# Performance work log

Measured on AMD Instinct MI355X. Metric: run time of the kernel, lower is better.

The kernel has to match this reference:

```python
import jax, jax.numpy as jnp
import numpy as np

B, E, H, N_TAYLOR = 8192, 256, 4096, 4
BN_EPS = 1e-5


def setup_inputs() -> dict:
    key = jax.random.key(0)
    ks = jax.random.split(key, 6)
    s = 0.02
    return {
        "z1": jax.random.normal(ks[0], (B, E), jnp.float32),
        "z2": jax.random.normal(ks[1], (B, E), jnp.float32),
        "p1": jax.random.normal(ks[2], (B, E), jnp.float32),
        "p2": jax.random.normal(ks[3], (B, E), jnp.float32),
        "W1": jax.random.normal(ks[4], (E, H), jnp.float32) * s,
        "gamma": jnp.ones((H,), jnp.float32),
        "beta": jnp.zeros((H,), jnp.float32),
        "W2": jax.random.normal(ks[5], (H, E), jnp.float32) * s,
        "b2": jnp.zeros((E,), jnp.float32),
        "lamda_inv": jnp.asarray(100.0, jnp.float32),
    }


def _predictor(z, W1, gamma, beta, W2, b2):
    h = z @ W1                                   # [B, H]
    mu = jnp.mean(h, axis=0)
    var = jnp.mean(jnp.square(h - mu), axis=0)   # biased var (torch BN training)
    h = (h - mu) * jax.lax.rsqrt(var + BN_EPS) * gamma + beta
    h = jax.nn.relu(h)
    return h @ W2 + b2                           # [B, E]


def _l2norm(x):
    n = jnp.linalg.norm(x, axis=1, keepdims=True)
    return x / jnp.maximum(n, 1e-12)


def _mec(view1, view2, lamda_inv):
    v1, v2 = _l2norm(view1), _l2norm(view2)
    c = (v1 @ v2.T) / lamda_inv                  # [B, B]
    power = c
    sum_p = jnp.zeros_like(c)
    for k in range(1, N_TAYLOR + 1):
        if k > 1:
            power = power @ c
        sign = 1.0 if (k + 1) % 2 == 0 else -1.0
        sum_p = sum_p + sign * power / k
    return jnp.trace(sum_p)


def reference(z1, z2, p1, p2, W1, gamma, beta, W2, b2, lamda_inv):
    q1 = _predictor(z1, W1, gamma, beta, W2, b2)
    q2 = _predictor(z2, W1, gamma, beta, W2, b2)
    loss = (_mec(p1, q2, lamda_inv) + _mec(p2, q1, lamda_inv)) * 0.5 / B
    return -loss * lamda_inv
```

## Files before the change

### kernel.cpp

```cpp
#include <hip/hip_runtime.h>

#define B_ROWS 8192
#define E_DIM  256
#define H_DIM  4096

typedef __attribute__((ext_vector_type(8))) short short8;
typedef __attribute__((ext_vector_type(4))) float f32x4;

typedef __attribute__((address_space(1))) const void* gas1_t;
typedef __attribute__((address_space(3))) void*       las3_t;

__device__ __forceinline__ float b2f(unsigned short s) {
    return __uint_as_float(((unsigned)s) << 16);
}
__device__ __forceinline__ unsigned short f2b(float f) {
    unsigned u = __float_as_uint(f);
    u += 0x7fffu + ((u >> 16) & 1u);
    return (unsigned short)(u >> 16);
}

__device__ __forceinline__ int swz(int row, int slot) {
    return slot ^ ((row >> 1) & 3);
}

__global__ void k_transpose_cast(const float* __restrict__ in,
                                 unsigned short* __restrict__ out,
                                 int R, int C) {
    __shared__ float tile[32][33];
    const int c0 = blockIdx.x * 32, r0 = blockIdx.y * 32;
    const int tx = threadIdx.x & 31, ty = threadIdx.x >> 5;
#pragma unroll
    for (int j = 0; j < 4; ++j)
        tile[ty * 4 + j][tx] = in[(size_t)(r0 + ty * 4 + j) * C + c0 + tx];
    __syncthreads();
#pragma unroll
    for (int j = 0; j < 4; ++j)
        out[(size_t)(c0 + ty * 4 + j) * R + r0 + tx] = f2b(tile[tx][ty * 4 + j]);
}

__global__ void k_cast_bf16(const float* __restrict__ in,
                            unsigned short* __restrict__ out, int n4) {
    int i = blockIdx.x * blockDim.x + threadIdx.x;
    if (i < n4) {
        float4 v = ((const float4*)in)[i];
        ushort4 o;
        o.x = f2b(v.x); o.y = f2b(v.y); o.z = f2b(v.z); o.w = f2b(v.w);
        ((ushort4*)out)[i] = o;
    }
}

__global__ __launch_bounds__(256) void k_gemm1(
    const unsigned short* __restrict__ A, const unsigned short* __restrict__ Bt,
    unsigned short* __restrict__ Cout,
    float* __restrict__ cs, float* __restrict__ cs2,
    int M, int N, int K) {
    constexpr int BK = 32, BM = 128, BN = 128;
    constexpr int MI = 4, NI = 4;
    __shared__ __align__(16) short As[BM * BK];
    __shared__ __align__(16) short Bs[BN * BK];

    const int t = threadIdx.x;
    const int lane = t & 63, wv = t >> 6;
    const int wr = wv >> 1, wc = wv & 1;
    const int l15 = lane & 15, quad = lane >> 4;
    const int m0 = blockIdx.y * BM, n0 = blockIdx.x * BN;

    f32x4 acc[MI][NI] = {};

    for (int k0 = 0; k0 < K; k0 += BK) {
#pragma unroll
        for (int q = 0; q < 2; ++q) {
            int u = q * 256 + t;
            int row = u >> 2, kc = swz(row, u & 3);
            const short* gp = (const short*)A + (size_t)(m0 + row) * K + k0 + kc * 8;
            short* lp = As + (size_t)(q * 256 + (wv << 6)) * 8;
            __builtin_amdgcn_global_load_lds((gas1_t)gp, (las3_t)lp, 16, 0, 0);
        }
#pragma unroll
        for (int q = 0; q < 2; ++q) {
            int u = q * 256 + t;
            int row = u >> 2, kc = swz(row, u & 3);
            const short* gp = (const short*)Bt + (size_t)(n0 + row) * K + k0 + kc * 8;
            short* lp = Bs + (size_t)(q * 256 + (wv << 6)) * 8;
            __builtin_amdgcn_global_load_lds((gas1_t)gp, (las3_t)lp, 16, 0, 0);
        }
        __syncthreads();

        short8 af[MI], bfr[NI];
#pragma unroll
        for (int mi = 0; mi < MI; ++mi) {
            int row = wr * 64 + mi * 16 + l15;
            af[mi] = *(const short8*)(As + row * BK + (swz(row, quad) << 3));
        }
#pragma unroll
        for (int ni = 0; ni < NI; ++ni) {
            int row = wc * 64 + ni * 16 + l15;
            bfr[ni] = *(const short8*)(Bs + row * BK + (swz(row, quad) << 3));
        }
#pragma unroll
        for (int mi = 0; mi < MI; ++mi)
#pragma unroll
            for (int ni = 0; ni < NI; ++ni)
                acc[mi][ni] = __builtin_amdgcn_mfma_f32_16x16x32_bf16(
                    af[mi], bfr[ni], acc[mi][ni], 0, 0, 0);
        __syncthreads();
    }

#pragma unroll
    for (int ni = 0; ni < NI; ++ni) {
        float s = 0.f, s2 = 0.f;
#pragma unroll
        for (int mi = 0; mi < MI; ++mi)
#pragma unroll
            for (int r = 0; r < 4; ++r) {
                int row = m0 + wr * 64 + mi * 16 + quad * 4 + r;
                int col = n0 + wc * 64 + ni * 16 + l15;
                float v = acc[mi][ni][r];
                Cout[(size_t)row * N + col] = f2b(v);
                s += v; s2 += v * v;
            }
        s  += __shfl_xor(s, 16);  s  += __shfl_xor(s, 32);
        s2 += __shfl_xor(s2, 16); s2 += __shfl_xor(s2, 32);
        if (quad == 0) {
            int col = n0 + wc * 64 + ni * 16 + l15;
            atomicAdd(&cs[col], s);
            atomicAdd(&cs2[col], s2);
        }
    }
}

__global__ void k_bnprep(const float* __restrict__ sum, const float* __restrict__ sumsq,
                         const float* __restrict__ gamma, const float* __restrict__ beta,
                         float* __restrict__ scale, float* __restrict__ shift) {
    int j = blockIdx.x * 256 + threadIdx.x;
    float mu = sum[j] * (1.f / B_ROWS);
    float var = sumsq[j] * (1.f / B_ROWS) - mu * mu;
    float sc = gamma[j] * rsqrtf(var + 1e-5f);
    scale[j] = sc;
    shift[j] = beta[j] - mu * sc;
}

__global__ __launch_bounds__(256) void k_gemm2f(
    const unsigned short* __restrict__ A, const unsigned short* __restrict__ Bt,
    float* __restrict__ Cout, const float* __restrict__ bias,
    const float* __restrict__ scale, const float* __restrict__ shift,
    int M, int N, int K) {
    constexpr int BK = 32, BM = 64, BN = 128;
    constexpr int MI = 2, NI = 4;
    __shared__ __align__(16) short As[BM * BK];
    __shared__ __align__(16) short Bs[BN * BK];

    const int t = threadIdx.x;
    const int lane = t & 63, wv = t >> 6;
    const int wr = wv >> 1, wc = wv & 1;
    const int l15 = lane & 15, quad = lane >> 4;
    const int m0 = blockIdx.y * BM, n0 = blockIdx.x * BN;

    const int Kc = K / gridDim.z;
    const int kbeg = blockIdx.z * Kc, kend = kbeg + Kc;

    const int arow = t >> 2, akc = t & 3;
    const unsigned short* hp = A + (size_t)(m0 + arow) * K + akc * 8;
    short* awp = As + arow * BK + (swz(arow, akc) << 3);
    const float* scp = scale + akc * 8;
    const float* shp = shift + akc * 8;

    f32x4 acc[MI][NI] = {};

    uint4 hreg; float4 sc0, sc1, sh0, sh1;
    {
        hreg = *(const uint4*)(hp + kbeg);
        sc0 = *(const float4*)(scp + kbeg); sc1 = *(const float4*)(scp + kbeg + 4);
        sh0 = *(const float4*)(shp + kbeg); sh1 = *(const float4*)(shp + kbeg + 4);
    }

    for (int k0 = kbeg; k0 < kend; k0 += BK) {
#pragma unroll
        for (int q = 0; q < 2; ++q) {
            int u = q * 256 + t;
            int row = u >> 2, kc = swz(row, u & 3);
            const short* gp = (const short*)Bt + (size_t)(n0 + row) * K + k0 + kc * 8;
            short* lp = Bs + (size_t)(q * 256 + (wv << 6)) * 8;
            __builtin_amdgcn_global_load_lds((gas1_t)gp, (las3_t)lp, 16, 0, 0);
        }

        uint4 cur = hreg;
        float sarr[8] = {sc0.x, sc0.y, sc0.z, sc0.w, sc1.x, sc1.y, sc1.z, sc1.w};
        float harr[8] = {sh0.x, sh0.y, sh0.z, sh0.w, sh1.x, sh1.y, sh1.z, sh1.w};
        if (k0 + BK < kend) {
            hreg = *(const uint4*)(hp + k0 + BK);
            sc0 = *(const float4*)(scp + k0 + BK); sc1 = *(const float4*)(scp + k0 + BK + 4);
            sh0 = *(const float4*)(shp + k0 + BK); sh1 = *(const float4*)(shp + k0 + BK + 4);
        }
        const unsigned short* hu = (const unsigned short*)&cur;
        short8 packed;
#pragma unroll
        for (int j = 0; j < 8; ++j) {
            float v = fmaxf(b2f(hu[j]) * sarr[j] + harr[j], 0.f);
            packed[j] = (short)f2b(v);
        }
        *(short8*)awp = packed;
        __syncthreads();

        short8 af[MI], bfr[NI];
#pragma unroll
        for (int mi = 0; mi < MI; ++mi) {
            int row = wr * 32 + mi * 16 + l15;
            af[mi] = *(const short8*)(As + row * BK + (swz(row, quad) << 3));
        }
#pragma unroll
        for (int ni = 0; ni < NI; ++ni) {
            int row = wc * 64 + ni * 16 + l15;
            bfr[ni] = *(const short8*)(Bs + row * BK + (swz(row, quad) << 3));
        }
#pragma unroll
        for (int mi = 0; mi < MI; ++mi)
#pragma unroll
            for (int ni = 0; ni < NI; ++ni)
                acc[mi][ni] = __builtin_amdgcn_mfma_f32_16x16x32_bf16(
                    af[mi], bfr[ni], acc[mi][ni], 0, 0, 0);
        __syncthreads();
    }

#pragma unroll
    for (int mi = 0; mi < MI; ++mi)
#pragma unroll
        for (int ni = 0; ni < NI; ++ni)
#pragma unroll
            for (int r = 0; r < 4; ++r) {
                int row = m0 + wr * 32 + mi * 16 + quad * 4 + r;
                int col = n0 + wc * 64 + ni * 16 + l15;
                float v = acc[mi][ni][r];
                if (blockIdx.z == 0) v += bias[col];
                atomicAdd(&Cout[(size_t)row * N + col], v);
            }
}

__global__ void k_rownorm4(const float* __restrict__ a0, const float* __restrict__ a1,
                           const float* __restrict__ a2, const float* __restrict__ a3,
                           float* __restrict__ o0, float* __restrict__ o1,
                           float* __restrict__ o2, float* __restrict__ o3) {
    int which = blockIdx.y;
    const float* x = which == 0 ? a0 : which == 1 ? a1 : which == 2 ? a2 : a3;
    float* inv = which == 0 ? o0 : which == 1 ? o1 : which == 2 ? o2 : o3;
    int row = blockIdx.x * 4 + (threadIdx.x >> 6);
    int lane = threadIdx.x & 63;
    float4 v = ((const float4*)(x + (size_t)row * E_DIM))[lane];
    float s = v.x * v.x + v.y * v.y + v.z * v.z + v.w * v.w;
#pragma unroll
    for (int o = 32; o; o >>= 1) s += __shfl_down(s, o);
    if (lane == 0) inv[row] = 1.f / fmaxf(sqrtf(s), 1e-12f);
}

__global__ void k_tn_cast(
    const float* __restrict__ x0, const float* __restrict__ x1,
    const float* __restrict__ x2, const float* __restrict__ x3,
    const float* __restrict__ i0, const float* __restrict__ i1,
    const float* __restrict__ i2, const float* __restrict__ i3,
    unsigned short* __restrict__ o0, unsigned short* __restrict__ o1,
    unsigned short* __restrict__ o2, unsigned short* __restrict__ o3) {
    const int z = blockIdx.z;
    const float* x = z == 0 ? x0 : z == 1 ? x1 : z == 2 ? x2 : x3;
    const float* inv = z == 0 ? i0 : z == 1 ? i1 : z == 2 ? i2 : i3;
    unsigned short* out = z == 0 ? o0 : z == 1 ? o1 : z == 2 ? o2 : o3;

    __shared__ float tile[32][33];
    const int c0 = blockIdx.x * 32, r0 = blockIdx.y * 32;
    const int tx = threadIdx.x & 31, ty = threadIdx.x >> 5;
#pragma unroll
    for (int j = 0; j < 4; ++j) {
        int r = r0 + ty * 4 + j;
        tile[ty * 4 + j][tx] = x[(size_t)r * E_DIM + c0 + tx] * inv[r];
    }
    __syncthreads();
#pragma unroll
    for (int j = 0; j < 4; ++j)
        out[(size_t)(c0 + ty * 4 + j) * B_ROWS + r0 + tx] = f2b(tile[tx][ty * 4 + j]);
}

#define GKS 16
__global__ __launch_bounds__(256) void k_gram(
    const unsigned short* __restrict__ p1T, const unsigned short* __restrict__ q2T,
    const unsigned short* __restrict__ p2T, const unsigned short* __restrict__ q1T,
    float* __restrict__ Ma, float* __restrict__ Mb) {
    constexpr int BK = 32;
    const int mec = blockIdx.z >> 4, kz = blockIdx.z & 15;
    const unsigned short* A = mec ? p2T : p1T;
    const unsigned short* Bt = mec ? q1T : q2T;
    float* Mout = mec ? Mb : Ma;

    __shared__ __align__(16) short As[64 * BK];
    __shared__ __align__(16) short Bs[64 * BK];

    const int t = threadIdx.x;
    const int lane = t & 63, wv = t >> 6;
    const int wr = wv >> 1, wc = wv & 1;
    const int l15 = lane & 15, quad = lane >> 4;
    const int m0 = blockIdx.y * 64, n0 = blockIdx.x * 64;
    const int kbeg = kz * (B_ROWS / GKS);

    f32x4 acc[2][2] = {};

    for (int k0 = kbeg; k0 < kbeg + B_ROWS / GKS; k0 += BK) {
        {
            int row = t >> 2, kc = swz(row, t & 3);
            const short* gpa = (const short*)A + (size_t)(m0 + row) * B_ROWS + k0 + kc * 8;
            short* lpa = As + (size_t)(wv << 6) * 8;
            __builtin_amdgcn_global_load_lds((gas1_t)gpa, (las3_t)lpa, 16, 0, 0);
            const short* gpb = (const short*)Bt + (size_t)(n0 + row) * B_ROWS + k0 + kc * 8;
            short* lpb = Bs + (size_t)(wv << 6) * 8;
            __builtin_amdgcn_global_load_lds((gas1_t)gpb, (las3_t)lpb, 16, 0, 0);
        }
        __syncthreads();

        short8 af[2], bfr[2];
#pragma unroll
        for (int mi = 0; mi < 2; ++mi) {
            int row = wr * 32 + mi * 16 + l15;
            af[mi] = *(const short8*)(As + row * BK + (swz(row, quad) << 3));
        }
#pragma unroll
        for (int ni = 0; ni < 2; ++ni) {
            int row = wc * 32 + ni * 16 + l15;
            bfr[ni] = *(const short8*)(Bs + row * BK + (swz(row, quad) << 3));
        }
#pragma unroll
        for (int mi = 0; mi < 2; ++mi)
#pragma unroll
            for (int ni = 0; ni < 2; ++ni)
                acc[mi][ni] = __builtin_amdgcn_mfma_f32_16x16x32_bf16(
                    af[mi], bfr[ni], acc[mi][ni], 0, 0, 0);
        __syncthreads();
    }

#pragma unroll
    for (int mi = 0; mi < 2; ++mi)
#pragma unroll
        for (int ni = 0; ni < 2; ++ni)
#pragma unroll
            for (int r = 0; r < 4; ++r) {
                int row = m0 + wr * 32 + mi * 16 + quad * 4 + r;
                int col = n0 + wc * 32 + ni * 16 + l15;
                atomicAdd(&Mout[(size_t)row * E_DIM + col], acc[mi][ni][r]);
            }
}

__global__ void k_m2(const float* __restrict__ Ma, const float* __restrict__ Mb,
                     float* __restrict__ M2a, float* __restrict__ M2b) {
    const float* M = blockIdx.z ? Mb : Ma;
    float* M2 = blockIdx.z ? M2b : M2a;
    int b = blockIdx.x * 16 + (threadIdx.x & 15);
    int a = blockIdx.y * 16 + (threadIdx.x >> 4);
    float s = 0.f;
    for (int k = 0; k < E_DIM; ++k) s += M[a * E_DIM + k] * M[k * E_DIM + b];
    M2[a * E_DIM + b] = s;
}

__global__ __launch_bounds__(256) void k_traces2(
    const float* __restrict__ Ma, const float* __restrict__ M2a,
    const float* __restrict__ Mb, const float* __restrict__ M2b,
    const float* __restrict__ lam, float* __restrict__ out) {
    const float* M  = blockIdx.z ? Mb  : Ma;
    const float* M2 = blockIdx.z ? M2b : M2a;
    const int i0 = blockIdx.y * 32, j0 = blockIdx.x * 32;
    const int t = threadIdx.x, col = t & 31, row = t >> 5;

    __shared__ float A[32][33], Bt[32][33], A2[32][33], B2[32][33];
#pragma unroll
    for (int r = 0; r < 4; ++r) {
        int rr = r * 8 + row;
        A [rr][col] = M [(i0 + rr) * E_DIM + j0 + col];
        Bt[rr][col] = M [(j0 + rr) * E_DIM + i0 + col];
        A2[rr][col] = M2[(i0 + rr) * E_DIM + j0 + col];
        B2[rr][col] = M2[(j0 + rr) * E_DIM + i0 + col];
    }
    __syncthreads();

    float lamv = lam[0];
    float il = 1.f / lamv;
    float F = -0.5f * lamv * (1.f / B_ROWS);
    float c1 = F * il;
    float c2 = -F * 0.5f * il * il;
    float c3 = F * (1.f / 3.f) * il * il * il;
    float c4 = -F * 0.25f * il * il * il * il;

    float s = 0.f;
#pragma unroll
    for (int r = 0; r < 4; ++r) {
        int rr = r * 8 + row;
        float mij = A[rr][col], mji = Bt[col][rr];
        float m2ij = A2[rr][col], m2ji = B2[col][rr];
        s += c2 * mij * mji + c3 * m2ij * mji + c4 * m2ij * m2ji;
        if (i0 + rr == j0 + col) s += c1 * mij;
    }
#pragma unroll
    for (int o = 32; o; o >>= 1) s += __shfl_down(s, o);
    __shared__ float red[4];
    if ((t & 63) == 0) red[t >> 6] = s;
    __syncthreads();
    if (t == 0) atomicAdd(out, red[0] + red[1] + red[2] + red[3]);
}

extern "C" void kernel_launch(void* const* d_in, const int* in_sizes, int n_in,
                              void* d_out, int out_size, void* d_ws, size_t ws_size,
                              hipStream_t stream) {
    const float* z1 = (const float*)d_in[0];
    const float* z2 = (const float*)d_in[1];
    const float* p1 = (const float*)d_in[2];
    const float* p2 = (const float*)d_in[3];
    const float* W1 = (const float*)d_in[4];
    const float* gamma = (const float*)d_in[5];
    const float* beta = (const float*)d_in[6];
    const float* W2 = (const float*)d_in[7];
    const float* b2 = (const float*)d_in[8];
    const float* lam = (const float*)d_in[9];
    float* out = (float*)d_out;
    char* ws = (char*)d_ws;

    size_t off = 0;
    auto alloc = [&](size_t bytes) { size_t o = off; off += (bytes + 255) & ~(size_t)255; return o; };
    unsigned short* W1T = (unsigned short*)(ws + alloc((size_t)E_DIM * H_DIM * 2));
    unsigned short* W2T = (unsigned short*)(ws + alloc((size_t)H_DIM * E_DIM * 2));
    unsigned short* zb  = (unsigned short*)(ws + alloc((size_t)B_ROWS * E_DIM * 2));
    unsigned short* h   = (unsigned short*)(ws + alloc((size_t)B_ROWS * H_DIM * 2));
    float* q1 = (float*)(ws + alloc((size_t)B_ROWS * E_DIM * 4));
    float* q2 = (float*)(ws + alloc((size_t)B_ROWS * E_DIM * 4));
    float* colsum   = (float*)(ws + alloc(H_DIM * 4));
    float* colsumsq = (float*)(ws + alloc(H_DIM * 4));
    float* scale = (float*)(ws + alloc(H_DIM * 4));
    float* shift = (float*)(ws + alloc(H_DIM * 4));
    float* invp1 = (float*)(ws + alloc(B_ROWS * 4));
    float* invp2 = (float*)(ws + alloc(B_ROWS * 4));
    float* invq1 = (float*)(ws + alloc(B_ROWS * 4));
    float* invq2 = (float*)(ws + alloc(B_ROWS * 4));
    float* Ma  = (float*)(ws + alloc((size_t)E_DIM * E_DIM * 4));
    float* Mb  = (float*)(ws + alloc((size_t)E_DIM * E_DIM * 4));
    float* M2a = (float*)(ws + alloc((size_t)E_DIM * E_DIM * 4));
    float* M2b = (float*)(ws + alloc((size_t)E_DIM * E_DIM * 4));

    const size_t TSZ = (size_t)E_DIM * B_ROWS;
    unsigned short* p1T = h;
    unsigned short* q2T = h + TSZ;
    unsigned short* p2T = h + 2 * TSZ;
    unsigned short* q1T = h + 3 * TSZ;

    hipMemsetAsync(out, 0, sizeof(float), stream);
    hipMemsetAsync(q1, 0, (size_t)2 * B_ROWS * E_DIM * sizeof(float), stream);

    k_transpose_cast<<<dim3(H_DIM / 32, E_DIM / 32), 256, 0, stream>>>(W1, W1T, E_DIM, H_DIM);
    k_transpose_cast<<<dim3(E_DIM / 32, H_DIM / 32), 256, 0, stream>>>(W2, W2T, H_DIM, E_DIM);

    const float* zs[2] = {z1, z2};
    float* qs[2] = {q1, q2};
    for (int v = 0; v < 2; ++v) {
        k_cast_bf16<<<dim3(B_ROWS * E_DIM / 4 / 256), 256, 0, stream>>>(zs[v], zb, B_ROWS * E_DIM / 4);
        hipMemsetAsync(colsum, 0, H_DIM * 2 * sizeof(float), stream);
        k_gemm1<<<dim3(H_DIM / 128, B_ROWS / 128), 256, 0, stream>>>(
            zb, W1T, h, colsum, colsumsq, B_ROWS, H_DIM, E_DIM);
        k_bnprep<<<dim3(H_DIM / 256), 256, 0, stream>>>(colsum, colsumsq, gamma, beta, scale, shift);
        k_gemm2f<<<dim3(E_DIM / 128, B_ROWS / 64, 4), 256, 0, stream>>>(
            h, W2T, qs[v], b2, scale, shift, B_ROWS, E_DIM, H_DIM);
    }

    k_rownorm4<<<dim3(B_ROWS / 4, 4), 256, 0, stream>>>(p1, p2, q1, q2, invp1, invp2, invq1, invq2);

    k_tn_cast<<<dim3(E_DIM / 32, B_ROWS / 32, 4), 256, 0, stream>>>(
        p1, q2, p2, q1, invp1, invq2, invp2, invq1, p1T, q2T, p2T, q1T);

    hipMemsetAsync(Ma, 0, (size_t)E_DIM * E_DIM * 2 * sizeof(float), stream);
    k_gram<<<dim3(4, 4, 2 * GKS), 256, 0, stream>>>(p1T, q2T, p2T, q1T, Ma, Mb);
    k_m2<<<dim3(16, 16, 2), 256, 0, stream>>>(Ma, Mb, M2a, M2b);
    k_traces2<<<dim3(8, 8, 2), 256, 0, stream>>>(Ma, M2a, Mb, M2b, lam, out);
}
```

Measured before the change: 351.8 us.

## Compute predictor output transposed, pack BN scale/shift as bf16, enlarge gram tiles

The second predictor GEMM now computes q transposed (W2T × h^T) with 128x128 tiles, writing directly into an E×B layout. The separate transpose-cast pass for q1/q2 is replaced by a column-norm plus a vectorized scale-and-cast kernel. BN scale and shift are packed into one bf16 pair per column, halving those loads at some precision cost. The gram kernel moves to 128x128 tiles with a deeper K split, which changes atomic traffic and occupancy.

```diff
diff --git a/kernel.cpp b/kernel.cpp
--- a/kernel.cpp
+++ b/kernel.cpp
@@ -131,118 +131,162 @@
 
 __global__ void k_bnprep(const float* __restrict__ sum, const float* __restrict__ sumsq,
                          const float* __restrict__ gamma, const float* __restrict__ beta,
-                         float* __restrict__ scale, float* __restrict__ shift) {
+                         unsigned* __restrict__ ssb) {
     int j = blockIdx.x * 256 + threadIdx.x;
     float mu = sum[j] * (1.f / B_ROWS);
     float var = sumsq[j] * (1.f / B_ROWS) - mu * mu;
     float sc = gamma[j] * rsqrtf(var + 1e-5f);
-    scale[j] = sc;
-    shift[j] = beta[j] - mu * sc;
-}
-
-__global__ __launch_bounds__(256) void k_gemm2f(
-    const unsigned short* __restrict__ A, const unsigned short* __restrict__ Bt,
-    float* __restrict__ Cout, const float* __restrict__ bias,
-    const float* __restrict__ scale, const float* __restrict__ shift,
-    int M, int N, int K) {
-    constexpr int BK = 32, BM = 64, BN = 128;
-    constexpr int MI = 2, NI = 4;
-    __shared__ __align__(16) short As[BM * BK];
-    __shared__ __align__(16) short Bs[BN * BK];
+    float sh = beta[j] - mu * sc;
+    ssb[j] = ((unsigned)f2b(sc) << 16) | (unsigned)f2b(sh);
+}
+
+__device__ __forceinline__ short8 bnrelu8(uint4 hv, uint4 sa, uint4 sb) {
+    const unsigned short* hu = (const unsigned short*)&hv;
+    const unsigned* wa = (const unsigned*)&sa;
+    const unsigned* wb = (const unsigned*)&sb;
+    short8 o;
+#pragma unroll
+    for (int j = 0; j < 8; ++j) {
+        unsigned w = j < 4 ? wa[j] : wb[j - 4];
+        float sc = __uint_as_float(w & 0xffff0000u);
+        float sh = __uint_as_float(w << 16);
+        float v = fmaxf(b2f(hu[j]) * sc + sh, 0.f);
+        o[j] = (short)f2b(v);
+    }
+    return o;
+}
+
+__global__ __launch_bounds__(256) void k_gemm2t(
+    const unsigned short* __restrict__ A, const unsigned short* __restrict__ H,
+    float* __restrict__ qT, const float* __restrict__ bias,
+    const unsigned* __restrict__ ssb, int K) {
+    constexpr int BK = 32;
+    __shared__ __align__(16) short As[128 * BK];
+    __shared__ __align__(16) short Bs[128 * BK];
 
     const int t = threadIdx.x;
     const int lane = t & 63, wv = t >> 6;
     const int wr = wv >> 1, wc = wv & 1;
     const int l15 = lane & 15, quad = lane >> 4;
-    const int m0 = blockIdx.y * BM, n0 = blockIdx.x * BN;
+    const int m0 = blockIdx.y * 128, n0 = blockIdx.x * 128;
 
     const int Kc = K / gridDim.z;
     const int kbeg = blockIdx.z * Kc, kend = kbeg + Kc;
 
-    const int arow = t >> 2, akc = t & 3;
-    const unsigned short* hp = A + (size_t)(m0 + arow) * K + akc * 8;
-    short* awp = As + arow * BK + (swz(arow, akc) << 3);
-    const float* scp = scale + akc * 8;
-    const float* shp = shift + akc * 8;
-
-    f32x4 acc[MI][NI] = {};
-
-    uint4 hreg; float4 sc0, sc1, sh0, sh1;
-    {
-        hreg = *(const uint4*)(hp + kbeg);
-        sc0 = *(const float4*)(scp + kbeg); sc1 = *(const float4*)(scp + kbeg + 4);
-        sh0 = *(const float4*)(shp + kbeg); sh1 = *(const float4*)(shp + kbeg + 4);
-    }
+    const int r0 = t >> 2, s0 = t & 3;
+    const int kc0 = swz(r0, s0);
+    const int kc1 = swz(64 + r0, s0);
+    const unsigned short* hp0 = H + (size_t)(n0 + r0) * K + kc0 * 8;
+    const unsigned short* hp1 = H + (size_t)(n0 + 64 + r0) * K + kc1 * 8;
+    short* bwp0 = Bs + r0 * BK + s0 * 8;
+    short* bwp1 = Bs + (64 + r0) * BK + s0 * 8;
+
+    f32x4 acc[4][4] = {};
+
+    uint4 hv0 = *(const uint4*)(hp0 + kbeg);
+    uint4 hv1 = *(const uint4*)(hp1 + kbeg);
 
     for (int k0 = kbeg; k0 < kend; k0 += BK) {
 #pragma unroll
         for (int q = 0; q < 2; ++q) {
             int u = q * 256 + t;
             int row = u >> 2, kc = swz(row, u & 3);
-            const short* gp = (const short*)Bt + (size_t)(n0 + row) * K + k0 + kc * 8;
-            short* lp = Bs + (size_t)(q * 256 + (wv << 6)) * 8;
+            const short* gp = (const short*)A + (size_t)(m0 + row) * K + k0 + kc * 8;
+            short* lp = As + (size_t)(q * 256 + (wv << 6)) * 8;
             __builtin_amdgcn_global_load_lds((gas1_t)gp, (las3_t)lp, 16, 0, 0);
         }
-
-        uint4 cur = hreg;
-        float sarr[8] = {sc0.x, sc0.y, sc0.z, sc0.w, sc1.x, sc1.y, sc1.z, sc1.w};
-        float harr[8] = {sh0.x, sh0.y, sh0.z, sh0.w, sh1.x, sh1.y, sh1.z, sh1.w};
+        uint4 sa0 = *(const uint4*)(ssb + k0 + kc0 * 8);
+        uint4 sa1 = *(const uint4*)(ssb + k0 + kc0 * 8 + 4);
+        uint4 sb0 = *(const uint4*)(ssb + k0 + kc1 * 8);
+        uint4 sb1 = *(const uint4*)(ssb + k0 + kc1 * 8 + 4);
+        uint4 c0 = hv0, c1 = hv1;
         if (k0 + BK < kend) {
-            hreg = *(const uint4*)(hp + k0 + BK);
-            sc0 = *(const float4*)(scp + k0 + BK); sc1 = *(const float4*)(scp + k0 + BK + 4);
-            sh0 = *(const float4*)(shp + k0 + BK); sh1 = *(const float4*)(shp + k0 + BK + 4);
-        }
-        const unsigned short* hu = (const unsigned short*)&cur;
-        short8 packed;
-#pragma unroll
-        for (int j = 0; j < 8; ++j) {
-            float v = fmaxf(b2f(hu[j]) * sarr[j] + harr[j], 0.f);
-            packed[j] = (short)f2b(v);
-        }
-        *(short8*)awp = packed;
+            hv0 = *(const uint4*)(hp0 + k0 + BK);
+            hv1 = *(const uint4*)(hp1 + k0 + BK);
+        }
+        *(short8*)bwp0 = bnrelu8(c0, sa0, sa1);
+        *(short8*)bwp1 = bnrelu8(c1, sb0, sb1);
         __syncthreads();
 
-        short8 af[MI], bfr[NI];
-#pragma unroll
-        for (int mi = 0; mi < MI; ++mi) {
-            int row = wr * 32 + mi * 16 + l15;
+        short8 af[4], bfr[4];
+#pragma unroll
+        for (int mi = 0; mi < 4; ++mi) {
+            int row = wr * 64 + mi * 16 + l15;
             af[mi] = *(const short8*)(As + row * BK + (swz(row, quad) << 3));
         }
 #pragma unroll
-        for (int ni = 0; ni < NI; ++ni) {
+        for (int ni = 0; ni < 4; ++ni) {
             int row = wc * 64 + ni * 16 + l15;
             bfr[ni] = *(const short8*)(Bs + row * BK + (swz(row, quad) << 3));
         }
 #pragma unroll
-        for (int mi = 0; mi < MI; ++mi)
-#pragma unroll
-            for (int ni = 0; ni < NI; ++ni)
+        for (int mi = 0; mi < 4; ++mi)
+#pragma unroll
+            for (int ni = 0; ni < 4; ++ni)
                 acc[mi][ni] = __builtin_amdgcn_mfma_f32_16x16x32_bf16(
                     af[mi], bfr[ni], acc[mi][ni], 0, 0, 0);
         __syncthreads();
     }
 
 #pragma unroll
-    for (int mi = 0; mi < MI; ++mi)
-#pragma unroll
-        for (int ni = 0; ni < NI; ++ni)
+    for (int mi = 0; mi < 4; ++mi)
+#pragma unroll
+        for (int ni = 0; ni < 4; ++ni)
 #pragma unroll
             for (int r = 0; r < 4; ++r) {
-                int row = m0 + wr * 32 + mi * 16 + quad * 4 + r;
+                int row = m0 + wr * 64 + mi * 16 + quad * 4 + r;
                 int col = n0 + wc * 64 + ni * 16 + l15;
                 float v = acc[mi][ni][r];
-                if (blockIdx.z == 0) v += bias[col];
-                atomicAdd(&Cout[(size_t)row * N + col], v);
+                if (blockIdx.z == 0) v += bias[row];
+                atomicAdd(&qT[(size_t)row * B_ROWS + col], v);
             }
 }
 
-__global__ void k_rownorm4(const float* __restrict__ a0, const float* __restrict__ a1,
-                           const float* __restrict__ a2, const float* __restrict__ a3,
-                           float* __restrict__ o0, float* __restrict__ o1,
-                           float* __restrict__ o2, float* __restrict__ o3) {
-    int which = blockIdx.y;
-    const float* x = which == 0 ? a0 : which == 1 ? a1 : which == 2 ? a2 : a3;
-    float* inv = which == 0 ? o0 : which == 1 ? o1 : which == 2 ? o2 : o3;
+__global__ void k_colnorm(const float* __restrict__ in0, const float* __restrict__ in1,
+                          float* __restrict__ inv0, float* __restrict__ inv1) {
+    const float* in = blockIdx.y ? in1 : in0;
+    float* invp = blockIdx.y ? inv1 : inv0;
+    const int cl = threadIdx.x & 63, rg = threadIdx.x >> 6;
+    const int col = blockIdx.x * 64 + cl;
+    float s = 0.f;
+    for (int e = rg * 64; e < rg * 64 + 64; ++e) {
+        float v = in[(size_t)e * B_ROWS + col];
+        s += v * v;
+    }
+    __shared__ float red[4][64];
+    red[rg][cl] = s;
+    __syncthreads();
+    if (rg == 0) {
+        float tot = red[0][cl] + red[1][cl] + red[2][cl] + red[3][cl];
+        invp[col] = 1.f / fmaxf(sqrtf(tot), 1e-12f);
+    }
+}
+
+__global__ void k_qscale(const float* __restrict__ in0, const float* __restrict__ in1,
+                         const float* __restrict__ inv0, const float* __restrict__ inv1,
+                         unsigned short* __restrict__ o0, unsigned short* __restrict__ o1) {
+    const float* in = blockIdx.y ? in1 : in0;
+    const float* inv = blockIdx.y ? inv1 : inv0;
+    unsigned short* outp = blockIdx.y ? o1 : o0;
+    size_t i8 = (size_t)blockIdx.x * 256 + threadIdx.x;
+    int row = (int)(i8 >> 10);
+    int col = (int)(i8 & 1023) * 8;
+    const float* p = in + (size_t)row * B_ROWS + col;
+    float4 a = ((const float4*)p)[0], b = ((const float4*)p)[1];
+    float4 ia = *(const float4*)(inv + col), ib = *(const float4*)(inv + col + 4);
+    ushort4 lo, hi;
+    lo.x = f2b(a.x * ia.x); lo.y = f2b(a.y * ia.y);
+    lo.z = f2b(a.z * ia.z); lo.w = f2b(a.w * ia.w);
+    hi.x = f2b(b.x * ib.x); hi.y = f2b(b.y * ib.y);
+    hi.z = f2b(b.z * ib.z); hi.w = f2b(b.w * ib.w);
+    ((ushort4*)(outp + (size_t)row * B_ROWS + col))[0] = lo;
+    ((ushort4*)(outp + (size_t)row * B_ROWS + col))[1] = hi;
+}
+
+__global__ void k_rownorm2(const float* __restrict__ a0, const float* __restrict__ a1,
+                           float* __restrict__ o0, float* __restrict__ o1) {
+    const float* x = blockIdx.y ? a1 : a0;
+    float* inv = blockIdx.y ? o1 : o0;
     int row = blockIdx.x * 4 + (threadIdx.x >> 6);
     int lane = threadIdx.x & 63;
     float4 v = ((const float4*)(x + (size_t)row * E_DIM))[lane];
@@ -254,15 +298,12 @@
 
 __global__ void k_tn_cast(
     const float* __restrict__ x0, const float* __restrict__ x1,
-    const float* __restrict__ x2, const float* __restrict__ x3,
     const float* __restrict__ i0, const float* __restrict__ i1,
-    const float* __restrict__ i2, const float* __restrict__ i3,
-    unsigned short* __restrict__ o0, unsigned short* __restrict__ o1,
-    unsigned short* __restrict__ o2, unsigned short* __restrict__ o3) {
+    unsigned short* __restrict__ o0, unsigned short* __restrict__ o1) {
     const int z = blockIdx.z;
-    const float* x = z == 0 ? x0 : z == 1 ? x1 : z == 2 ? x2 : x3;
-    const float* inv = z == 0 ? i0 : z == 1 ? i1 : z == 2 ? i2 : i3;
-    unsigned short* out = z == 0 ? o0 : z == 1 ? o1 : z == 2 ? o2 : o3;
+    const float* x = z ? x1 : x0;
+    const float* inv = z ? i1 : i0;
+    unsigned short* out = z ? o1 : o0;
 
     __shared__ float tile[32][33];
     const int c0 = blockIdx.x * 32, r0 = blockIdx.y * 32;
@@ -278,69 +319,76 @@
         out[(size_t)(c0 + ty * 4 + j) * B_ROWS + r0 + tx] = f2b(tile[tx][ty * 4 + j]);
 }
 
-#define GKS 16
-__global__ __launch_bounds__(256) void k_gram(
+#define GKS 32
+__global__ __launch_bounds__(256) void k_gram2(
     const unsigned short* __restrict__ p1T, const unsigned short* __restrict__ q2T,
     const unsigned short* __restrict__ p2T, const unsigned short* __restrict__ q1T,
     float* __restrict__ Ma, float* __restrict__ Mb) {
     constexpr int BK = 32;
-    const int mec = blockIdx.z >> 4, kz = blockIdx.z & 15;
+    const int mec = blockIdx.z >> 5, kz = blockIdx.z & 31;
     const unsigned short* A = mec ? p2T : p1T;
     const unsigned short* Bt = mec ? q1T : q2T;
     float* Mout = mec ? Mb : Ma;
 
-    __shared__ __align__(16) short As[64 * BK];
-    __shared__ __align__(16) short Bs[64 * BK];
+    __shared__ __align__(16) short As[128 * BK];
+    __shared__ __align__(16) short Bs[128 * BK];
 
     const int t = threadIdx.x;
     const int lane = t & 63, wv = t >> 6;
     const int wr = wv >> 1, wc = wv & 1;
     const int l15 = lane & 15, quad = lane >> 4;
-    const int m0 = blockIdx.y * 64, n0 = blockIdx.x * 64;
+    const int m0 = blockIdx.y * 128, n0 = blockIdx.x * 128;
     const int kbeg = kz * (B_ROWS / GKS);
 
-    f32x4 acc[2][2] = {};
+    f32x4 acc[4][4] = {};
 
     for (int k0 = kbeg; k0 < kbeg + B_ROWS / GKS; k0 += BK) {
-        {
-            int row = t >> 2, kc = swz(row, t & 3);
-            const short* gpa = (const short*)A + (size_t)(m0 + row) * B_ROWS + k0 + kc * 8;
-            short* lpa = As + (size_t)(wv << 6) * 8;
-            __builtin_amdgcn_global_load_lds((gas1_t)gpa, (las3_t)lpa, 16, 0, 0);
-            const short* gpb = (const short*)Bt + (size_t)(n0 + row) * B_ROWS + k0 + kc * 8;
-            short* lpb = Bs + (size_t)(wv << 6) * 8;
-            __builtin_amdgcn_global_load_lds((gas1_t)gpb, (las3_t)lpb, 16, 0, 0);
+#pragma unroll
+        for (int q = 0; q < 2; ++q) {
+            int u = q * 256 + t;
+            int row = u >> 2, kc = swz(row, u & 3);
+            const short* gp = (const short*)A + (size_t)(m0 + row) * B_ROWS + k0 + kc * 8;
+            short* lp = As + (size_t)(q * 256 + (wv << 6)) * 8;
+            __builtin_amdgcn_global_load_lds((gas1_t)gp, (las3_t)lp, 16, 0, 0);
+        }
+#pragma unroll
+        for (int q = 0; q < 2; ++q) {
+            int u = q * 256 + t;
+            int row = u >> 2, kc = swz(row, u & 3);
+            const short* gp = (const short*)Bt + (size_t)(n0 + row) * B_ROWS + k0 + kc * 8;
+            short* lp = Bs + (size_t)(q * 256 + (wv << 6)) * 8;
+            __builtin_amdgcn_global_load_lds((gas1_t)gp, (las3_t)lp, 16, 0, 0);
         }
         __syncthreads();
 
-        short8 af[2], bfr[2];
-#pragma unroll
-        for (int mi = 0; mi < 2; ++mi) {
-            int row = wr * 32 + mi * 16 + l15;
+        short8 af[4], bfr[4];
+#pragma unroll
+        for (int mi = 0; mi < 4; ++mi) {
+            int row = wr * 64 + mi * 16 + l15;
             af[mi] = *(const short8*)(As + row * BK + (swz(row, quad) << 3));
         }
 #pragma unroll
-        for (int ni = 0; ni < 2; ++ni) {
-            int row = wc * 32 + ni * 16 + l15;
+        for (int ni = 0; ni < 4; ++ni) {
+            int row = wc * 64 + ni * 16 + l15;
             bfr[ni] = *(const short8*)(Bs + row * BK + (swz(row, quad) << 3));
         }
 #pragma unroll
-        for (int mi = 0; mi < 2; ++mi)
-#pragma unroll
-            for (int ni = 0; ni < 2; ++ni)
+        for (int mi = 0; mi < 4; ++mi)
+#pragma unroll
+            for (int ni = 0; ni < 4; ++ni)
                 acc[mi][ni] = __builtin_amdgcn_mfma_f32_16x16x32_bf16(
                     af[mi], bfr[ni], acc[mi][ni], 0, 0, 0);
         __syncthreads();
     }
 
 #pragma unroll
-    for (int mi = 0; mi < 2; ++mi)
-#pragma unroll
-        for (int ni = 0; ni < 2; ++ni)
+    for (int mi = 0; mi < 4; ++mi)
+#pragma unroll
+        for (int ni = 0; ni < 4; ++ni)
 #pragma unroll
             for (int r = 0; r < 4; ++r) {
-                int row = m0 + wr * 32 + mi * 16 + quad * 4 + r;
-                int col = n0 + wc * 32 + ni * 16 + l15;
+                int row = m0 + wr * 64 + mi * 16 + quad * 4 + r;
+                int col = n0 + wc * 64 + ni * 16 + l15;
                 atomicAdd(&Mout[(size_t)row * E_DIM + col], acc[mi][ni][r]);
             }
 }
@@ -423,12 +471,11 @@
     unsigned short* W2T = (unsigned short*)(ws + alloc((size_t)H_DIM * E_DIM * 2));
     unsigned short* zb  = (unsigned short*)(ws + alloc((size_t)B_ROWS * E_DIM * 2));
     unsigned short* h   = (unsigned short*)(ws + alloc((size_t)B_ROWS * H_DIM * 2));
-    float* q1 = (float*)(ws + alloc((size_t)B_ROWS * E_DIM * 4));
-    float* q2 = (float*)(ws + alloc((size_t)B_ROWS * E_DIM * 4));
+    float* qT1f = (float*)(ws + alloc((size_t)E_DIM * B_ROWS * 4));
+    float* qT2f = (float*)(ws + alloc((size_t)E_DIM * B_ROWS * 4));
     float* colsum   = (float*)(ws + alloc(H_DIM * 4));
     float* colsumsq = (float*)(ws + alloc(H_DIM * 4));
-    float* scale = (float*)(ws + alloc(H_DIM * 4));
-    float* shift = (float*)(ws + alloc(H_DIM * 4));
+    unsigned* ssb = (unsigned*)(ws + alloc(H_DIM * 4));
     float* invp1 = (float*)(ws + alloc(B_ROWS * 4));
     float* invp2 = (float*)(ws + alloc(B_ROWS * 4));
     float* invq1 = (float*)(ws + alloc(B_ROWS * 4));
@@ -440,35 +487,38 @@
 
     const size_t TSZ = (size_t)E_DIM * B_ROWS;
     unsigned short* p1T = h;
-    unsigned short* q2T = h + TSZ;
-    unsigned short* p2T = h + 2 * TSZ;
-    unsigned short* q1T = h + 3 * TSZ;
+    unsigned short* p2T = h + TSZ;
+    unsigned short* q1T = h + 2 * TSZ;
+    unsigned short* q2T = h + 3 * TSZ;
 
     hipMemsetAsync(out, 0, sizeof(float), stream);
-    hipMemsetAsync(q1, 0, (size_t)2 * B_ROWS * E_DIM * sizeof(float), stream);
+    hipMemsetAsync(qT1f, 0, (size_t)2 * E_DIM * B_ROWS * sizeof(float), stream);
 
     k_transpose_cast<<<dim3(H_DIM / 32, E_DIM / 32), 256, 0, stream>>>(W1, W1T, E_DIM, H_DIM);
     k_transpose_cast<<<dim3(E_DIM / 32, H_DIM / 32), 256, 0, stream>>>(W2, W2T, H_DIM, E_DIM);
 
     const float* zs[2] = {z1, z2};
-    float* qs[2] = {q1, q2};
+    float* qTs[2] = {qT1f, qT2f};
     for (int v = 0; v < 2; ++v) {
         k_cast_bf16<<<dim3(B_ROWS * E_DIM / 4 / 256), 256, 0, stream>>>(zs[v], zb, B_ROWS * E_DIM / 4);
         hipMemsetAsync(colsum, 0, H_DIM * 2 * sizeof(float), stream);
         k_gemm1<<<dim3(H_DIM / 128, B_ROWS / 128), 256, 0, stream>>>(
             zb, W1T, h, colsum, colsumsq, B_ROWS, H_DIM, E_DIM);
-        k_bnprep<<<dim3(H_DIM / 256), 256, 0, stream>>>(colsum, colsumsq, gamma, beta, scale, shift);
-        k_gemm2f<<<dim3(E_DIM / 128, B_ROWS / 64, 4), 256, 0, stream>>>(
-            h, W2T, qs[v], b2, scale, shift, B_ROWS, E_DIM, H_DIM);
-    }
-
-    k_rownorm4<<<dim3(B_ROWS / 4, 4), 256, 0, stream>>>(p1, p2, q1, q2, invp1, invp2, invq1, invq2);
-
-    k_tn_cast<<<dim3(E_DIM / 32, B_ROWS / 32, 4), 256, 0, stream>>>(
-        p1, q2, p2, q1, invp1, invq2, invp2, invq1, p1T, q2T, p2T, q1T);
+        k_bnprep<<<dim3(H_DIM / 256), 256, 0, stream>>>(colsum, colsumsq, gamma, beta, ssb);
+        k_gemm2t<<<dim3(B_ROWS / 128, E_DIM / 128, 4), 256, 0, stream>>>(
+            W2T, h, qTs[v], b2, ssb, H_DIM);
+    }
+
+    k_rownorm2<<<dim3(B_ROWS / 4, 2), 256, 0, stream>>>(p1, p2, invp1, invp2);
+    k_tn_cast<<<dim3(E_DIM / 32, B_ROWS / 32, 2), 256, 0, stream>>>(
+        p1, p2, invp1, invp2, p1T, p2T);
+
+    k_colnorm<<<dim3(B_ROWS / 64, 2), 256, 0, stream>>>(qT1f, qT2f, invq1, invq2);
+    k_qscale<<<dim3(E_DIM * B_ROWS / 8 / 256, 2), 256, 0, stream>>>(
+        qT1f, qT2f, invq1, invq2, q1T, q2T);
 
     hipMemsetAsync(Ma, 0, (size_t)E_DIM * E_DIM * 2 * sizeof(float), stream);
-    k_gram<<<dim3(4, 4, 2 * GKS), 256, 0, stream>>>(p1T, q2T, p2T, q1T, Ma, Mb);
+    k_gram2<<<dim3(2, 2, 2 * GKS), 256, 0, stream>>>(p1T, q2T, p2T, q1T, Ma, Mb);
     k_m2<<<dim3(16, 16, 2), 256, 0, stream>>>(Ma, Mb, M2a, M2b);
     k_traces2<<<dim3(8, 8, 2), 256, 0, stream>>>(Ma, M2a, Mb, M2b, lam, out);
 }
```

Result: slower. 402.3 us (+14.3%).
